# Kernel optimization log

Measured on AMD Instinct MI355X. Metric: run time of the kernel, lower is better.

## Reference

```python
import jax, jax.numpy as jnp
import numpy as np

B, S, IN, N, MOT = 128, 4096, 6, 64, 3
ODE_UNFOLDS = 6
EPS = 1e-8


def setup_inputs() -> dict:
    ks = jax.random.split(jax.random.key(0), 20)
    u = lambda k, shape, lo, hi: jax.random.uniform(k, shape, jnp.float32, lo, hi)
    pm1 = lambda k, shape: jnp.where(jax.random.bernoulli(k, 0.5, shape), 1.0, -1.0).astype(jnp.float32)
    return {
        "x": jax.random.normal(ks[0], (B, S, IN), jnp.float32),
        "mean_us": 0.1 * jax.random.normal(ks[1], (IN,), jnp.float32),
        "std_us": u(ks[2], (IN,), 0.5, 1.5),
        "input_w": u(ks[3], (IN,), 0.8, 1.2),
        "input_b": 0.01 * jax.random.normal(ks[4], (IN,), jnp.float32),
        "output_w": u(ks[5], (MOT,), 0.8, 1.2),
        "output_b": 0.01 * jax.random.normal(ks[6], (MOT,), jnp.float32),
        "gleak": u(ks[7], (N,), 0.001, 1.0),
        "vleak": u(ks[8], (N,), -0.2, 0.2),
        "cm": u(ks[9], (N,), 0.4, 0.6),
        "sensory_W": u(ks[10], (IN, N), 0.001, 1.0),
        "sensory_mu": u(ks[11], (IN, N), 0.3, 0.8),
        "sensory_sigma": u(ks[12], (IN, N), 3.0, 8.0),
        "sensory_erev": pm1(ks[13], (IN, N)),
        "W": u(ks[14], (N, N), 0.001, 1.0),
        "mu": u(ks[15], (N, N), 0.3, 0.8),
        "sigma": u(ks[16], (N, N), 3.0, 8.0),
        "erev": pm1(ks[17], (N, N)),
    }


def _ltc_sequence(x, mean_us, std_us, input_w, input_b, output_w, output_b,
                  gleak, vleak, cm, sensory_W, sensory_mu, sensory_sigma,
                  sensory_erev, W, mu, sigma, erev):
    # normalize inputs (DgaRawSequence) then LTCCell input mapping
    xn = (x - mean_us) / std_us                      # [B,S,IN]
    xm = xn * input_w + input_b                      # [B,S,IN]
    cm_t = cm * ODE_UNFOLDS                          # cm / (elapsed_time=1 / ode_unfolds)

    def step(v, u_t):                                # v: [B,N], u_t: [B,IN]
        # sensory synapse activations [B,IN,N]
        s_act = sensory_W * jax.nn.sigmoid((u_t[:, :, None] - sensory_mu) * sensory_sigma)
        wns = jnp.sum(s_act * sensory_erev, axis=1)  # [B,N]
        wds = jnp.sum(s_act, axis=1)                 # [B,N]
        for _ in range(ODE_UNFOLDS):
            w_act = W * jax.nn.sigmoid((v[:, :, None] - mu) * sigma)  # [B,N,N]
            num = cm_t * v + gleak * vleak + jnp.sum(w_act * erev, axis=1) + wns
            den = cm_t + gleak + jnp.sum(w_act, axis=1) + wds
            v = num / (den + EPS)
        return v, v

    v0 = jnp.zeros((x.shape[0], gleak.shape[0]), dtype=x.dtype)
    _, vs = jax.lax.scan(step, v0, jnp.swapaxes(xm, 0, 1))   # [S,B,N]
    states = jnp.swapaxes(vs, 0, 1)                          # [B,S,N]
    # LTCCell output mapping (motor neurons = first MOT states)
    out = states[..., :MOT] * output_w + output_b            # [B,S,3]
    # denormalize (DgaRawSequence)
    return out * std_us[:MOT] + mean_us[:MOT]


def reference(x, mean_us, std_us, input_w, input_b, output_w, output_b,
              gleak, vleak, cm, sensory_W, sensory_mu, sensory_sigma,
              sensory_erev, W, mu, sigma, erev):
    return _ltc_sequence(x, mean_us, std_us, input_w, input_b, output_w,
                         output_b, gleak, vleak, cm, sensory_W, sensory_mu,
                         sensory_sigma, sensory_erev, W, mu, sigma, erev)
```

## Files before the change

kernel.cpp:

```cpp
#include <hip/hip_runtime.h>

#define B_ 128
#define S_ 4096
#define IN_ 6
#define N_ 64
#define MOT_ 3
#define UNF 6
#define EPS_ 1e-8f
#define LOG2E 1.4426950408889634f

__device__ __forceinline__ float red16(float x) {
#if __has_builtin(__builtin_amdgcn_permlane16_swap)
    auto r = __builtin_amdgcn_permlane16_swap(__float_as_int(x), __float_as_int(x),
                                              false, false);
    return __int_as_float((int)r[0]) + __int_as_float((int)r[1]);
#else
    return x + __shfl_xor(x, 16, 64);
#endif
}
__device__ __forceinline__ float red32(float x) {
#if __has_builtin(__builtin_amdgcn_permlane32_swap)
    auto r = __builtin_amdgcn_permlane32_swap(__float_as_int(x), __float_as_int(x),
                                              false, false);
    return __int_as_float((int)r[0]) + __int_as_float((int)r[1]);
#else
    return x + __shfl_xor(x, 32, 64);
#endif
}

__device__ __forceinline__ void lds_barrier() {
    asm volatile("s_waitcnt lgkmcnt(0)" ::: "memory");
    __builtin_amdgcn_s_barrier();
}

__launch_bounds__(256, 1)
__global__ void ltc_kernel(
    const float* __restrict__ x,
    const float* __restrict__ mean_us, const float* __restrict__ std_us,
    const float* __restrict__ input_w, const float* __restrict__ input_b,
    const float* __restrict__ output_w, const float* __restrict__ output_b,
    const float* __restrict__ gleak, const float* __restrict__ vleak,
    const float* __restrict__ cm,
    const float* __restrict__ sW, const float* __restrict__ sMu,
    const float* __restrict__ sSig, const float* __restrict__ sErev,
    const float* __restrict__ W, const float* __restrict__ Mu,
    const float* __restrict__ Sig, const float* __restrict__ Erev,
    float* __restrict__ out)
{
    const int b    = blockIdx.x;
    const int t    = threadIdx.x;
    const int lane = t & 63;
    const int w    = t >> 6;
    const int cc   = lane >> 4;
    const int ii   = lane & 15;
    const int myCol = w * 16 + ii;
    const int jb   = cc * 16;

    __shared__ __align__(16) float vbuf[2][N_];
    __shared__ float s_lds[IN_][N_][2];

    float A[16], Bc[16], Wr[16], We[16];
#pragma unroll
    for (int jj = 0; jj < 16; ++jj) {
        int idx = (jb + jj) * N_ + myCol;
        float sg = Sig[idx], m = Mu[idx], ww = W[idx], e = Erev[idx];
        A[jj]  = -sg * LOG2E;
        Bc[jj] = m * sg * LOG2E;
        Wr[jj] = ww;
        We[jj] = ww * e;
    }

    const float cmt = cm[myCol] * (float)UNF;
    const float glk = gleak[myCol];
    const float gv  = glk * vleak[myCol];
    const float dbase = cmt + glk + EPS_;

    const int i0 = w;
    const int i1 = w + 4;
    const bool has1 = (w < 2);
    float SA0, SB0, SWv0, SWe0, ns0, nb0;
    {
        int idx = i0 * N_ + lane;
        float sg = sSig[idx], m = sMu[idx], ww = sW[idx], e = sErev[idx];
        SA0 = -sg * LOG2E; SB0 = m * sg * LOG2E; SWv0 = ww; SWe0 = ww * e;
        ns0 = input_w[i0] / std_us[i0];
        nb0 = input_b[i0] - mean_us[i0] / std_us[i0] * input_w[i0];
    }
    float SA1 = 0.f, SB1 = 0.f, SWv1 = 0.f, SWe1 = 0.f, ns1 = 0.f, nb1 = 0.f;
    if (has1) {
        int idx = i1 * N_ + lane;
        float sg = sSig[idx], m = sMu[idx], ww = sW[idx], e = sErev[idx];
        SA1 = -sg * LOG2E; SB1 = m * sg * LOG2E; SWv1 = ww; SWe1 = ww * e;
        ns1 = input_w[i1] / std_us[i1];
        nb1 = input_b[i1] - mean_us[i1] / std_us[i1] * input_w[i1];
    }

    float OW = 0.f, OB = 0.f;
    if (t < MOT_) {
        OW = output_w[t] * std_us[t];
        OB = output_b[t] * std_us[t] + mean_us[t];
    }

    const float* xb = x + (size_t)b * S_ * IN_;
    float* ob = out + (size_t)b * S_ * MOT_;

    if (t < N_) vbuf[0][t] = 0.f;
    {
        float u  = fmaf(xb[i0], ns0, nb0);
        float e  = __builtin_amdgcn_exp2f(fmaf(u, SA0, SB0));
        float sg = __builtin_amdgcn_rcpf(1.0f + e);
        s_lds[i0][lane][0] = SWe0 * sg;
        s_lds[i0][lane][1] = SWv0 * sg;
        if (has1) {
            float u1  = fmaf(xb[i1], ns1, nb1);
            float e1  = __builtin_amdgcn_exp2f(fmaf(u1, SA1, SB1));
            float sg1 = __builtin_amdgcn_rcpf(1.0f + e1);
            s_lds[i1][lane][0] = SWe1 * sg1;
            s_lds[i1][lane][1] = SWv1 * sg1;
        }
    }
    lds_barrier();

    float v_my = 0.f;

    for (int s = 0; s < S_; ++s) {
        const int s1 = (s + 1 < S_) ? (s + 1) : s;
        float xn0 = xb[s1 * IN_ + i0];
        float xn1 = has1 ? xb[s1 * IN_ + i1] : 0.f;

        float a = 0.f, d = 0.f;
#pragma unroll
        for (int ci = 0; ci < IN_; ++ci) {
            float2 sv = *(const float2*)&s_lds[ci][myCol][0];
            a += sv.x; d += sv.y;
        }
        const float nb = gv + a;
        const float db = dbase + d;

#pragma unroll
        for (int k = 0; k < UNF; ++k) {
            const int p = k & 1;
            float4 v0 = *(const float4*)&vbuf[p][jb];
            float4 v1 = *(const float4*)&vbuf[p][jb + 4];
            float4 v2 = *(const float4*)&vbuf[p][jb + 8];
            float4 v3 = *(const float4*)&vbuf[p][jb + 12];
            const float vj[16] = {v0.x, v0.y, v0.z, v0.w, v1.x, v1.y, v1.z, v1.w,
                                  v2.x, v2.y, v2.z, v2.w, v3.x, v3.y, v3.z, v3.w};

            float pn = 0.f, pd = 0.f;
#pragma unroll
            for (int jj = 0; jj < 16; ++jj) {
                float e  = __builtin_amdgcn_exp2f(fmaf(vj[jj], A[jj], Bc[jj]));
                float sg = __builtin_amdgcn_rcpf(1.0f + e);
                pn = fmaf(We[jj], sg, pn);
                pd = fmaf(Wr[jj], sg, pd);
            }
            pn = red16(pn);  pd = red16(pd);
            pn = red32(pn);  pd = red32(pd);

            float num = fmaf(cmt, v_my, nb + pn);
            v_my = num * __builtin_amdgcn_rcpf(db + pd);

            if (cc == 0) vbuf[p ^ 1][myCol] = v_my;

            if (k == 1) {
                float u  = fmaf(xn0, ns0, nb0);
                float e2 = __builtin_amdgcn_exp2f(fmaf(u, SA0, SB0));
                float sg = __builtin_amdgcn_rcpf(1.0f + e2);
                s_lds[i0][lane][0] = SWe0 * sg;
                s_lds[i0][lane][1] = SWv0 * sg;
                if (has1) {
                    float u1  = fmaf(xn1, ns1, nb1);
                    float e3  = __builtin_amdgcn_exp2f(fmaf(u1, SA1, SB1));
                    float sg1 = __builtin_amdgcn_rcpf(1.0f + e3);
                    s_lds[i1][lane][0] = SWe1 * sg1;
                    s_lds[i1][lane][1] = SWv1 * sg1;
                }
            }
            lds_barrier();
        }

        if (t < MOT_) ob[s * MOT_ + t] = fmaf(v_my, OW, OB);
    }
}

extern "C" void kernel_launch(void* const* d_in, const int* in_sizes, int n_in,
                              void* d_out, int out_size, void* d_ws, size_t ws_size,
                              hipStream_t stream) {
    (void)in_sizes; (void)n_in; (void)d_ws; (void)ws_size; (void)out_size;
    const float* x       = (const float*)d_in[0];
    const float* mean_us = (const float*)d_in[1];
    const float* std_us  = (const float*)d_in[2];
    const float* input_w = (const float*)d_in[3];
    const float* input_b = (const float*)d_in[4];
    const float* out_w   = (const float*)d_in[5];
    const float* out_b   = (const float*)d_in[6];
    const float* gleak   = (const float*)d_in[7];
    const float* vleak   = (const float*)d_in[8];
    const float* cm      = (const float*)d_in[9];
    const float* sW      = (const float*)d_in[10];
    const float* sMu     = (const float*)d_in[11];
    const float* sSig    = (const float*)d_in[12];
    const float* sErev   = (const float*)d_in[13];
    const float* W       = (const float*)d_in[14];
    const float* Mu      = (const float*)d_in[15];
    const float* Sig     = (const float*)d_in[16];
    const float* Erev    = (const float*)d_in[17];
    float* out = (float*)d_out;

    ltc_kernel<<<dim3(B_), dim3(256), 0, stream>>>(
        x, mean_us, std_us, input_w, input_b, out_w, out_b,
        gleak, vleak, cm, sW, sMu, sSig, sErev, W, Mu, Sig, Erev, out);
}
```

Baseline: 9.593 ms.

## Process two batch rows per block to interleave independent recurrences

```diff
diff --git a/kernel.cpp b/kernel.cpp
--- a/kernel.cpp
+++ b/kernel.cpp
@@ -47,7 +47,6 @@
     const float* __restrict__ Sig, const float* __restrict__ Erev,
     float* __restrict__ out)
 {
-    const int b    = blockIdx.x;
     const int t    = threadIdx.x;
     const int lane = t & 63;
     const int w    = t >> 6;
@@ -56,8 +55,8 @@
     const int myCol = w * 16 + ii;
     const int jb   = cc * 16;
 
-    __shared__ __align__(16) float vbuf[2][N_];
-    __shared__ float s_lds[IN_][N_][2];
+    __shared__ __align__(16) float vbuf[2][2][N_];
+    __shared__ float s_lds[2][IN_][N_][2];
 
     float A[16], Bc[16], Wr[16], We[16];
 #pragma unroll
@@ -101,86 +100,124 @@
         OB = output_b[t] * std_us[t] + mean_us[t];
     }
 
-    const float* xb = x + (size_t)b * S_ * IN_;
-    float* ob = out + (size_t)b * S_ * MOT_;
-
-    if (t < N_) vbuf[0][t] = 0.f;
+    const int bA = blockIdx.x * 2;
+    const int bB = bA + 1;
+    const float* xA = x + (size_t)bA * S_ * IN_;
+    const float* xB = x + (size_t)bB * S_ * IN_;
+    float* oA = out + (size_t)bA * S_ * MOT_;
+    float* oB = out + (size_t)bB * S_ * MOT_;
+
+    if (t < N_) { vbuf[0][0][t] = 0.f; vbuf[0][1][t] = 0.f; }
     {
-        float u  = fmaf(xb[i0], ns0, nb0);
-        float e  = __builtin_amdgcn_exp2f(fmaf(u, SA0, SB0));
-        float sg = __builtin_amdgcn_rcpf(1.0f + e);
-        s_lds[i0][lane][0] = SWe0 * sg;
-        s_lds[i0][lane][1] = SWv0 * sg;
+        float uA = fmaf(xA[i0], ns0, nb0);
+        float uB = fmaf(xB[i0], ns0, nb0);
+        float eA = __builtin_amdgcn_exp2f(fmaf(uA, SA0, SB0));
+        float eB = __builtin_amdgcn_exp2f(fmaf(uB, SA0, SB0));
+        float sA = __builtin_amdgcn_rcpf(1.0f + eA);
+        float sB = __builtin_amdgcn_rcpf(1.0f + eB);
+        s_lds[0][i0][lane][0] = SWe0 * sA;  s_lds[0][i0][lane][1] = SWv0 * sA;
+        s_lds[1][i0][lane][0] = SWe0 * sB;  s_lds[1][i0][lane][1] = SWv0 * sB;
         if (has1) {
-            float u1  = fmaf(xb[i1], ns1, nb1);
-            float e1  = __builtin_amdgcn_exp2f(fmaf(u1, SA1, SB1));
-            float sg1 = __builtin_amdgcn_rcpf(1.0f + e1);
-            s_lds[i1][lane][0] = SWe1 * sg1;
-            s_lds[i1][lane][1] = SWv1 * sg1;
+            float uA1 = fmaf(xA[i1], ns1, nb1);
+            float uB1 = fmaf(xB[i1], ns1, nb1);
+            float eA1 = __builtin_amdgcn_exp2f(fmaf(uA1, SA1, SB1));
+            float eB1 = __builtin_amdgcn_exp2f(fmaf(uB1, SA1, SB1));
+            float sA1 = __builtin_amdgcn_rcpf(1.0f + eA1);
+            float sB1 = __builtin_amdgcn_rcpf(1.0f + eB1);
+            s_lds[0][i1][lane][0] = SWe1 * sA1;  s_lds[0][i1][lane][1] = SWv1 * sA1;
+            s_lds[1][i1][lane][0] = SWe1 * sB1;  s_lds[1][i1][lane][1] = SWv1 * sB1;
         }
     }
     lds_barrier();
 
-    float v_my = 0.f;
+    float vA = 0.f, vB = 0.f;
 
     for (int s = 0; s < S_; ++s) {
         const int s1 = (s + 1 < S_) ? (s + 1) : s;
-        float xn0 = xb[s1 * IN_ + i0];
-        float xn1 = has1 ? xb[s1 * IN_ + i1] : 0.f;
-
-        float a = 0.f, d = 0.f;
+        float xnA0 = xA[s1 * IN_ + i0];
+        float xnB0 = xB[s1 * IN_ + i0];
+        float xnA1 = has1 ? xA[s1 * IN_ + i1] : 0.f;
+        float xnB1 = has1 ? xB[s1 * IN_ + i1] : 0.f;
+
+        float aA = 0.f, dA = 0.f, aB = 0.f, dB = 0.f;
 #pragma unroll
         for (int ci = 0; ci < IN_; ++ci) {
-            float2 sv = *(const float2*)&s_lds[ci][myCol][0];
-            a += sv.x; d += sv.y;
-        }
-        const float nb = gv + a;
-        const float db = dbase + d;
+            float2 svA = *(const float2*)&s_lds[0][ci][myCol][0];
+            float2 svB = *(const float2*)&s_lds[1][ci][myCol][0];
+            aA += svA.x; dA += svA.y;
+            aB += svB.x; dB += svB.y;
+        }
+        const float nbA = gv + aA, dbA = dbase + dA;
+        const float nbB = gv + aB, dbB = dbase + dB;
 
 #pragma unroll
         for (int k = 0; k < UNF; ++k) {
             const int p = k & 1;
-            float4 v0 = *(const float4*)&vbuf[p][jb];
-            float4 v1 = *(const float4*)&vbuf[p][jb + 4];
-            float4 v2 = *(const float4*)&vbuf[p][jb + 8];
-            float4 v3 = *(const float4*)&vbuf[p][jb + 12];
-            const float vj[16] = {v0.x, v0.y, v0.z, v0.w, v1.x, v1.y, v1.z, v1.w,
-                                  v2.x, v2.y, v2.z, v2.w, v3.x, v3.y, v3.z, v3.w};
-
-            float pn = 0.f, pd = 0.f;
+            float4 a0 = *(const float4*)&vbuf[p][0][jb];
+            float4 a1 = *(const float4*)&vbuf[p][0][jb + 4];
+            float4 a2 = *(const float4*)&vbuf[p][0][jb + 8];
+            float4 a3 = *(const float4*)&vbuf[p][0][jb + 12];
+            float4 b0 = *(const float4*)&vbuf[p][1][jb];
+            float4 b1 = *(const float4*)&vbuf[p][1][jb + 4];
+            float4 b2 = *(const float4*)&vbuf[p][1][jb + 8];
+            float4 b3 = *(const float4*)&vbuf[p][1][jb + 12];
+            const float vjA[16] = {a0.x,a0.y,a0.z,a0.w, a1.x,a1.y,a1.z,a1.w,
+                                   a2.x,a2.y,a2.z,a2.w, a3.x,a3.y,a3.z,a3.w};
+            const float vjB[16] = {b0.x,b0.y,b0.z,b0.w, b1.x,b1.y,b1.z,b1.w,
+                                   b2.x,b2.y,b2.z,b2.w, b3.x,b3.y,b3.z,b3.w};
+
+            float pnA = 0.f, pdA = 0.f, pnB = 0.f, pdB = 0.f;
 #pragma unroll
             for (int jj = 0; jj < 16; ++jj) {
-                float e  = __builtin_amdgcn_exp2f(fmaf(vj[jj], A[jj], Bc[jj]));
-                float sg = __builtin_amdgcn_rcpf(1.0f + e);
-                pn = fmaf(We[jj], sg, pn);
-                pd = fmaf(Wr[jj], sg, pd);
+                float eA  = __builtin_amdgcn_exp2f(fmaf(vjA[jj], A[jj], Bc[jj]));
+                float eB  = __builtin_amdgcn_exp2f(fmaf(vjB[jj], A[jj], Bc[jj]));
+                float sgA = __builtin_amdgcn_rcpf(1.0f + eA);
+                float sgB = __builtin_amdgcn_rcpf(1.0f + eB);
+                pnA = fmaf(We[jj], sgA, pnA);
+                pdA = fmaf(Wr[jj], sgA, pdA);
+                pnB = fmaf(We[jj], sgB, pnB);
+                pdB = fmaf(Wr[jj], sgB, pdB);
             }
-            pn = red16(pn);  pd = red16(pd);
-            pn = red32(pn);  pd = red32(pd);
-
-            float num = fmaf(cmt, v_my, nb + pn);
-            v_my = num * __builtin_amdgcn_rcpf(db + pd);
-
-            if (cc == 0) vbuf[p ^ 1][myCol] = v_my;
+            pnA = red16(pnA);  pdA = red16(pdA);
+            pnB = red16(pnB);  pdB = red16(pdB);
+            pnA = red32(pnA);  pdA = red32(pdA);
+            pnB = red32(pnB);  pdB = red32(pdB);
+
+            vA = fmaf(cmt, vA, nbA + pnA) * __builtin_amdgcn_rcpf(dbA + pdA);
+            vB = fmaf(cmt, vB, nbB + pnB) * __builtin_amdgcn_rcpf(dbB + pdB);
+
+            if (cc == 0) {
+                vbuf[p ^ 1][0][myCol] = vA;
+                vbuf[p ^ 1][1][myCol] = vB;
+            }
 
             if (k == 1) {
-                float u  = fmaf(xn0, ns0, nb0);
-                float e2 = __builtin_amdgcn_exp2f(fmaf(u, SA0, SB0));
-                float sg = __builtin_amdgcn_rcpf(1.0f + e2);
-                s_lds[i0][lane][0] = SWe0 * sg;
-                s_lds[i0][lane][1] = SWv0 * sg;
+                float uA = fmaf(xnA0, ns0, nb0);
+                float uB = fmaf(xnB0, ns0, nb0);
+                float eA = __builtin_amdgcn_exp2f(fmaf(uA, SA0, SB0));
+                float eB = __builtin_amdgcn_exp2f(fmaf(uB, SA0, SB0));
+                float sA = __builtin_amdgcn_rcpf(1.0f + eA);
+                float sB = __builtin_amdgcn_rcpf(1.0f + eB);
+                s_lds[0][i0][lane][0] = SWe0 * sA;  s_lds[0][i0][lane][1] = SWv0 * sA;
+                s_lds[1][i0][lane][0] = SWe0 * sB;  s_lds[1][i0][lane][1] = SWv0 * sB;
                 if (has1) {
-                    float u1  = fmaf(xn1, ns1, nb1);
-                    float e3  = __builtin_amdgcn_exp2f(fmaf(u1, SA1, SB1));
-                    float sg1 = __builtin_amdgcn_rcpf(1.0f + e3);
-                    s_lds[i1][lane][0] = SWe1 * sg1;
-                    s_lds[i1][lane][1] = SWv1 * sg1;
+                    float uA1 = fmaf(xnA1, ns1, nb1);
+                    float uB1 = fmaf(xnB1, ns1, nb1);
+                    float eA1 = __builtin_amdgcn_exp2f(fmaf(uA1, SA1, SB1));
+                    float eB1 = __builtin_amdgcn_exp2f(fmaf(uB1, SA1, SB1));
+                    float sA1 = __builtin_amdgcn_rcpf(1.0f + eA1);
+                    float sB1 = __builtin_amdgcn_rcpf(1.0f + eB1);
+                    s_lds[0][i1][lane][0] = SWe1 * sA1;  s_lds[0][i1][lane][1] = SWv1 * sA1;
+                    s_lds[1][i1][lane][0] = SWe1 * sB1;  s_lds[1][i1][lane][1] = SWv1 * sB1;
                 }
             }
             lds_barrier();
         }
 
-        if (t < MOT_) ob[s * MOT_ + t] = fmaf(v_my, OW, OB);
+        if (t < MOT_) {
+            oA[s * MOT_ + t] = fmaf(vA, OW, OB);
+            oB[s * MOT_ + t] = fmaf(vB, OW, OB);
+        }
     }
 }
 
@@ -208,7 +245,7 @@
     const float* Erev    = (const float*)d_in[17];
     float* out = (float*)d_out;
 
-    ltc_kernel<<<dim3(B_), dim3(256), 0, stream>>>(
+    ltc_kernel<<<dim3(B_ / 2), dim3(256), 0, stream>>>(
         x, mean_us, std_us, input_w, input_b, out_w, out_b,
         gleak, vleak, cm, sW, sMu, sSig, sErev, W, Mu, Sig, Erev, out);
 }
```

Result: slower. 16.61 ms (+73.1%).
